# Optimization experiments

Measured on AMD Instinct MI355X. Metric: run time of the kernel, lower is better.

Reference implementation:

```python
import jax, jax.numpy as jnp
import numpy as np

B, H, L, D = 2, 16, 2048, 128


def setup_inputs() -> dict:
    key = jax.random.key(0)
    kq, kk, kv = jax.random.split(key, 3)
    q = jax.random.normal(kq, (B, H, L, D), dtype=jnp.float32)
    k = jax.random.normal(kk, (B, H, L, D), dtype=jnp.float32)
    v = jax.random.normal(kv, (B, H, L, D), dtype=jnp.float32)
    return {"q": q, "k": k, "v": v}


def reference(q, k, v):
    # Causal prefill attention (flash_attn_varlen_func / SDPA is_causal=True path).
    # q, k, v: [B, H, L, D]; scale = 1/sqrt(D) as in the fallback and constructor.
    Lq = q.shape[2]
    Dh = q.shape[3]
    scale = 1.0 / jnp.sqrt(jnp.asarray(Dh, q.dtype))
    scores = jnp.einsum('bhqd,bhkd->bhqk', q, k) * scale  # [B,H,Lq,Lk]
    causal = jnp.tril(jnp.ones((Lq, Lq), dtype=bool))      # [Lq,Lk]
    scores = jnp.where(causal, scores, jnp.finfo(q.dtype).min)
    probs = jax.nn.softmax(scores, axis=-1)
    return jnp.einsum('bhqk,bhkd->bhqd', probs, v)          # [B,H,Lq,D]
```

## Files before the change

kernel.cpp:

```cpp
#include <hip/hip_runtime.h>
#include <hip/hip_bf16.h>
#include <stdint.h>


#define BB 2
#define HH 16
#define LL 2048
#define DD 128

typedef float f32x4 __attribute__((ext_vector_type(4)));
typedef __bf16 bf16x8 __attribute__((ext_vector_type(8)));
typedef __bf16 bf16x2t __attribute__((ext_vector_type(2)));

union Frag16 {
    uint4    u;
    bf16x8   b;
    uint16_t s[8];
    uint32_t w32[4];
};

__device__ inline uint32_t pk2bf(float x, float y) {
    bf16x2t v;
    v.x = (__bf16)x;
    v.y = (__bf16)y;
    return __builtin_bit_cast(uint32_t, v);
}

__device__ inline uint16_t f2bf(float x) {
    uint32_t u = __builtin_bit_cast(uint32_t, x);
    u += 0x7fffu + ((u >> 16) & 1u);
    return (uint16_t)(u >> 16);
}

__device__ inline float fast_exp2(float x) {
#if __has_builtin(__builtin_amdgcn_exp2f)
    return __builtin_amdgcn_exp2f(x);
#else
    return exp2f(x);
#endif
}

__device__ __forceinline__ void stage16(const uint4* g, uint4* l) {
    __builtin_amdgcn_global_load_lds(
        (const __attribute__((address_space(1))) unsigned int*)g,
        (__attribute__((address_space(3))) unsigned int*)l, 16, 0, 0);
}

__global__ __launch_bounds__(256) void conv_kv(
    const float* __restrict__ Kg, const float* __restrict__ Vg,
    uint4* __restrict__ Kf, uint4* __restrict__ Vf)
{
    const int bid = blockIdx.x;
    const int t   = threadIdx.x;
    if (bid < 2048) {
        const int unit = bid;
        #pragma unroll
        for (int i = 0; i < 2; ++i) {
            const int local = t + i * 256;
            const int tile  = unit * 2 + (local >> 8);
            const int c     = local & 255;
            const int ds = c >> 6, quad = (c >> 4) & 3, n16 = c & 15;
            const float* p = Kg + ((size_t)tile * 16 + n16) * DD + ds * 32 + quad * 8;
            float4 a = *(const float4*)p;
            float4 b = *(const float4*)(p + 4);
            Frag16 f;
            f.w32[0] = pk2bf(a.x, a.y); f.w32[1] = pk2bf(a.z, a.w);
            f.w32[2] = pk2bf(b.x, b.y); f.w32[3] = pk2bf(b.z, b.w);
            Kf[(size_t)tile * 256 + c] = f.u;
        }
    } else {
        const int g = bid - 2048;
        const int n16 = t & 15, dt = (t >> 4) & 7, quadH = t >> 7;
        #pragma unroll
        for (int qi = 0; qi < 2; ++qi) {
            const int quad = quadH + 2 * qi;
            const float* base = Vg + ((size_t)g * 32 + quad * 8) * DD + dt * 16 + n16;
            float v[8];
            #pragma unroll
            for (int j = 0; j < 8; ++j) v[j] = base[(size_t)j * DD];
            Frag16 f;
            f.w32[0] = pk2bf(v[0], v[1]); f.w32[1] = pk2bf(v[2], v[3]);
            f.w32[2] = pk2bf(v[4], v[5]); f.w32[3] = pk2bf(v[6], v[7]);
            Vf[(size_t)g * 512 + dt * 64 + quad * 16 + n16] = f.u;
        }
    }
}

__global__ __launch_bounds__(256, 2) void fa_main(
    const float* __restrict__ Qg, const uint4* __restrict__ Kf,
    const uint4* __restrict__ Vf, float* __restrict__ Og)
{
    __shared__ __align__(16) uint4 Klds[2][512];
    __shared__ __align__(16) uint4 Vlds[2][512];
    __shared__ __align__(16) uint16_t Plds[4][16 * 40];

    const int tid  = threadIdx.x;
    const int lane = tid & 63;
    const int w    = tid >> 6;
    const int n16  = lane & 15;
    const int quad = lane >> 4;

    const int i    = blockIdx.x;
    const int xcd  = i & 7;
    const int j    = i >> 3;
    const int pair = j & 15;
    const int bh   = xcd * 4 + (j >> 4);

    constexpr float kC   = 0.08838834764831845f * 1.4426950408889634f;
    constexpr float kOff = -16.0f * 1.4426950408889634f;

    float* Oh = Og + (size_t)bh * LL * DD;

    const int kq_off = (w >> 1) * 256 + ((w & 1) * 2) * 64;
    const int vq_off = (2 * w) * 64;

    #pragma unroll
    for (int phase = 0; phase < 2; ++phase) {
        const int qtile  = phase ? pair : 31 - pair;
        const int q0     = qtile * 64;
        const int q_base = q0 + w * 16;

        Frag16 qf[4];
        {
            const float* qrow = Qg + ((size_t)bh * LL + q_base + n16) * DD;
            #pragma unroll
            for (int ds = 0; ds < 4; ++ds) {
                const int d0 = ds * 32 + quad * 8;
                float4 a = *(const float4*)(qrow + d0);
                float4 b = *(const float4*)(qrow + d0 + 4);
                qf[ds].w32[0] = pk2bf(a.x, a.y); qf[ds].w32[1] = pk2bf(a.z, a.w);
                qf[ds].w32[2] = pk2bf(b.x, b.y); qf[ds].w32[3] = pk2bf(b.z, b.w);
            }
        }

        f32x4 oacc[8];
        #pragma unroll
        for (int dt = 0; dt < 8; ++dt) oacc[dt] = (f32x4)0.0f;
        float lpart = 0.0f;

        const int nt = 2 * qtile + 2;

        {
            const uint4* kg = Kf + ((size_t)(bh * 128) * 256) + kq_off + lane;
            const uint4* vg = Vf + ((size_t)(bh * 64) * 512) + vq_off + lane;
            stage16(kg,      &Klds[0][kq_off]);
            stage16(kg + 64, &Klds[0][kq_off + 64]);
            stage16(vg,      &Vlds[0][vq_off]);
            stage16(vg + 64, &Vlds[0][vq_off + 64]);
        }
        __syncthreads();

        int cur = 0;
        for (int t = 0; t < nt; ++t) {
            if (t + 1 < nt) {
                const uint4* kg = Kf + ((size_t)(bh * 128 + 2 * (t + 1)) * 256) + kq_off + lane;
                const uint4* vg = Vf + ((size_t)(bh * 64 + (t + 1)) * 512) + vq_off + lane;
                uint4* kd = &Klds[cur ^ 1][kq_off];
                uint4* vd = &Vlds[cur ^ 1][vq_off];
                stage16(kg,      kd);
                stage16(kg + 64, kd + 64);
                stage16(vg,      vd);
                stage16(vg + 64, vd + 64);
            }

            const uint4* Kl = Klds[cur];
            const uint4* Vl = Vlds[cur];
            const int kv0 = t << 5;

            f32x4 sacc[2] = {(f32x4)0.0f, (f32x4)0.0f};
            Frag16 kf[2][4];
            #pragma unroll
            for (int kt = 0; kt < 2; ++kt)
                #pragma unroll
                for (int ds = 0; ds < 4; ++ds) kf[kt][ds].u = Kl[kt * 256 + ds * 64 + lane];
            __builtin_amdgcn_s_setprio(1);
            #pragma unroll
            for (int ds = 0; ds < 4; ++ds) {
                sacc[0] = __builtin_amdgcn_mfma_f32_16x16x32_bf16(kf[0][ds].b, qf[ds].b, sacc[0], 0, 0, 0);
                sacc[1] = __builtin_amdgcn_mfma_f32_16x16x32_bf16(kf[1][ds].b, qf[ds].b, sacc[1], 0, 0, 0);
            }
            __builtin_amdgcn_s_setprio(0);

            Frag16 vf[8];
            #pragma unroll
            for (int dt = 0; dt < 8; ++dt) vf[dt].u = Vl[dt * 64 + lane];

            if (kv0 + 31 > q_base) {
                const int qg_ = q_base + n16;
                #pragma unroll
                for (int kt = 0; kt < 2; ++kt) {
                    const int kvg = kv0 + kt * 16 + quad * 4;
                    #pragma unroll
                    for (int r = 0; r < 4; ++r)
                        if (kvg + r > qg_) sacc[kt][r] = -1e30f;
                }
            }

            #pragma unroll
            for (int kt = 0; kt < 2; ++kt) {
                float p0 = fast_exp2(fmaf(sacc[kt][0], kC, kOff));
                float p1 = fast_exp2(fmaf(sacc[kt][1], kC, kOff));
                float p2 = fast_exp2(fmaf(sacc[kt][2], kC, kOff));
                float p3 = fast_exp2(fmaf(sacc[kt][3], kC, kOff));
                lpart += (p0 + p1) + (p2 + p3);
                uint2 pw;
                pw.x = pk2bf(p0, p1);
                pw.y = pk2bf(p2, p3);
                *(uint2*)&Plds[w][n16 * 40 + kt * 16 + quad * 4] = pw;
            }

            Frag16 pf;
            pf.u = *(const uint4*)&Plds[w][n16 * 40 + quad * 8];
            __builtin_amdgcn_s_setprio(1);
            #pragma unroll
            for (int dt = 0; dt < 8; ++dt)
                oacc[dt] = __builtin_amdgcn_mfma_f32_16x16x32_bf16(
                    pf.b, vf[dt].b, oacc[dt], 0, 0, 0);
            __builtin_amdgcn_s_setprio(0);

            __syncthreads();
            cur ^= 1;
        }

        float lsum = lpart;
        lsum += __shfl_xor(lsum, 16);
        lsum += __shfl_xor(lsum, 32);
        #pragma unroll
        for (int r = 0; r < 4; ++r) {
            const float inv = 1.0f / __shfl(lsum, quad * 4 + r);
            float* orow = Oh + (size_t)(q_base + quad * 4 + r) * DD + n16;
            #pragma unroll
            for (int dt = 0; dt < 8; ++dt)
                orow[dt * 16] = oacc[dt][r] * inv;
        }
    }
}

__global__ __launch_bounds__(256) void fa_fallback(
    const float* __restrict__ Qg, const float* __restrict__ Kg,
    const float* __restrict__ Vg, float* __restrict__ Og)
{
    __shared__ uint4 Klds[32 * 16];
    __shared__ uint4 Vlds[128 * 4];
    __shared__ __align__(16) uint16_t Plds[4][32 * 40];

    const int tid  = threadIdx.x;
    const int lane = tid & 63;
    const int w    = tid >> 6;
    const int n16  = lane & 15;
    const int quad = lane >> 4;

    const int bh     = blockIdx.y;
    const int q0     = (gridDim.x - 1 - blockIdx.x) * 128;
    const int q_base = q0 + w * 32;

    const size_t base = (size_t)bh * LL * DD;
    const float* Qh = Qg + base;
    const float* Kh = Kg + base;
    const float* Vh = Vg + base;
    float*       Oh = Og + base;

    constexpr float kC = 0.08838834764831845f * 1.4426950408889634f;

    Frag16 qf[2][4];
    #pragma unroll
    for (int qt = 0; qt < 2; ++qt) {
        const float* qrow = Qh + (size_t)(q_base + qt * 16 + n16) * DD;
        #pragma unroll
        for (int ds = 0; ds < 4; ++ds) {
            const int d0 = ds * 32 + quad * 8;
            float4 a = *(const float4*)(qrow + d0);
            float4 b = *(const float4*)(qrow + d0 + 4);
            Frag16 f;
            f.s[0] = f2bf(a.x); f.s[1] = f2bf(a.y); f.s[2] = f2bf(a.z); f.s[3] = f2bf(a.w);
            f.s[4] = f2bf(b.x); f.s[5] = f2bf(b.y); f.s[6] = f2bf(b.z); f.s[7] = f2bf(b.w);
            qf[qt][ds] = f;
        }
    }

    f32x4 oacc[2][8];
    #pragma unroll
    for (int qt = 0; qt < 2; ++qt)
        #pragma unroll
        for (int dt = 0; dt < 8; ++dt) oacc[qt][dt] = (f32x4)0.0f;
    float mrow[2] = {-1e30f, -1e30f};
    float lrow[2] = {0.0f, 0.0f};

    const int ntiles = q0 / 32 + 4;

    for (int t = 0; t < ntiles; ++t) {
        const int kv0 = t * 32;
        __syncthreads();
        #pragma unroll
        for (int iu = 0; iu < 2; ++iu) {
            const int cid = tid + iu * 256;
            const int r = cid >> 4, c = cid & 15;
            const float* src = Kh + (size_t)(kv0 + r) * DD + c * 8;
            float4 a = *(const float4*)src;
            float4 b = *(const float4*)(src + 4);
            Frag16 f;
            f.s[0] = f2bf(a.x); f.s[1] = f2bf(a.y); f.s[2] = f2bf(a.z); f.s[3] = f2bf(a.w);
            f.s[4] = f2bf(b.x); f.s[5] = f2bf(b.y); f.s[6] = f2bf(b.z); f.s[7] = f2bf(b.w);
            Klds[r * 16 + (c ^ (r & 7))] = f.u;
        }
        #pragma unroll
        for (int iu = 0; iu < 2; ++iu) {
            const int cid = tid + iu * 256;
            const int d = cid >> 2, ch = cid & 3;
            const float* src = Vh + (size_t)(kv0 + ch * 8) * DD + d;
            Frag16 f;
            #pragma unroll
            for (int j = 0; j < 8; ++j) f.s[j] = f2bf(src[(size_t)j * DD]);
            Vlds[d * 4 + (ch ^ ((d >> 1) & 3))] = f.u;
        }
        __syncthreads();

        if (kv0 > q_base + 31) continue;

        f32x4 sacc[2][2];
        #pragma unroll
        for (int kt = 0; kt < 2; ++kt)
            #pragma unroll
            for (int qt = 0; qt < 2; ++qt) sacc[kt][qt] = (f32x4)0.0f;

        #pragma unroll
        for (int ds = 0; ds < 4; ++ds) {
            Frag16 kfr[2];
            #pragma unroll
            for (int kt = 0; kt < 2; ++kt) {
                const int r = kt * 16 + n16;
                const int c = ds * 4 + quad;
                kfr[kt].u = Klds[r * 16 + (c ^ (r & 7))];
            }
            #pragma unroll
            for (int kt = 0; kt < 2; ++kt)
                #pragma unroll
                for (int qt = 0; qt < 2; ++qt)
                    sacc[kt][qt] = __builtin_amdgcn_mfma_f32_16x16x32_bf16(
                        kfr[kt].b, qf[qt][ds].b, sacc[kt][qt], 0, 0, 0);
        }

        if (kv0 + 31 > q_base) {
            #pragma unroll
            for (int kt = 0; kt < 2; ++kt) {
                const int kvg = kv0 + kt * 16 + quad * 4;
                #pragma unroll
                for (int qt = 0; qt < 2; ++qt) {
                    const int qg_ = q_base + qt * 16 + n16;
                    #pragma unroll
                    for (int r = 0; r < 4; ++r)
                        if (kvg + r > qg_) sacc[kt][qt][r] = -1e30f;
                }
            }
        }

        #pragma unroll
        for (int qt = 0; qt < 2; ++qt) {
            float mt = sacc[0][qt][0];
            #pragma unroll
            for (int kt = 0; kt < 2; ++kt)
                #pragma unroll
                for (int r = 0; r < 4; ++r) mt = fmaxf(mt, sacc[kt][qt][r]);
            mt = fmaxf(mt, __shfl_xor(mt, 16));
            mt = fmaxf(mt, __shfl_xor(mt, 32));
            const float mnew  = fmaxf(mrow[qt], mt);
            const float alpha = exp2f((mrow[qt] - mnew) * kC);
            mrow[qt] = mnew;

            float ls = 0.0f;
            uint16_t* prow = &Plds[w][(qt * 16 + n16) * 40];
            #pragma unroll
            for (int kt = 0; kt < 2; ++kt)
                #pragma unroll
                for (int r = 0; r < 4; ++r) {
                    const float p = exp2f((sacc[kt][qt][r] - mnew) * kC);
                    ls += p;
                    prow[kt * 16 + quad * 4 + r] = f2bf(p);
                }
            ls += __shfl_xor(ls, 16);
            ls += __shfl_xor(ls, 32);
            lrow[qt] = lrow[qt] * alpha + ls;

            #pragma unroll
            for (int r = 0; r < 4; ++r) {
                const float ar = __shfl(alpha, quad * 4 + r);
                #pragma unroll
                for (int dt = 0; dt < 8; ++dt) oacc[qt][dt][r] *= ar;
            }
        }

        Frag16 pfr[2];
        #pragma unroll
        for (int qt = 0; qt < 2; ++qt)
            pfr[qt].u = *(const uint4*)&Plds[w][(qt * 16 + n16) * 40 + quad * 8];
        #pragma unroll
        for (int dt = 0; dt < 8; ++dt) {
            const int d = dt * 16 + n16;
            Frag16 vfr;
            vfr.u = Vlds[d * 4 + (quad ^ ((d >> 1) & 3))];
            #pragma unroll
            for (int qt = 0; qt < 2; ++qt)
                oacc[qt][dt] = __builtin_amdgcn_mfma_f32_16x16x32_bf16(
                    pfr[qt].b, vfr.b, oacc[qt][dt], 0, 0, 0);
        }
    }

    #pragma unroll
    for (int qt = 0; qt < 2; ++qt) {
        #pragma unroll
        for (int r = 0; r < 4; ++r) {
            const float lr  = __shfl(lrow[qt], quad * 4 + r);
            const float inv = 1.0f / lr;
            const int row = q_base + qt * 16 + quad * 4 + r;
            float* orow = Oh + (size_t)row * DD + n16;
            #pragma unroll
            for (int dt = 0; dt < 8; ++dt)
                orow[dt * 16] = oacc[qt][dt][r] * inv;
        }
    }
}

extern "C" void kernel_launch(void* const* d_in, const int* in_sizes, int n_in,
                              void* d_out, int out_size, void* d_ws, size_t ws_size,
                              hipStream_t stream) {
    const float* q = (const float*)d_in[0];
    const float* k = (const float*)d_in[1];
    const float* v = (const float*)d_in[2];
    float* o = (float*)d_out;

    const size_t TENS = (size_t)BB * HH * LL * DD * 2;
    if (ws_size >= 2 * TENS) {
        uint4* Kf = (uint4*)d_ws;
        uint4* Vf = (uint4*)((char*)d_ws + TENS);
        conv_kv<<<dim3(4096), dim3(256), 0, stream>>>(k, v, Kf, Vf);
        fa_main<<<dim3(512), dim3(256), 0, stream>>>(q, Kf, Vf, o);
    } else {
        fa_fallback<<<dim3(16, BB * HH), dim3(256), 0, stream>>>(q, k, v, o);
    }
}
```

Before: 185.0 us.

## Split KV range across two wave groups per block and merge partial outputs

Doubles the block to 512 threads, with two groups of four waves each processing alternating 32-key halves of a 64-key stage. Partial output accumulators and row sums are merged through shared memory, reusing the K buffer, before the final store. Tiles that lie fully above the causal diagonal are now skipped per wave. This raises parallelism per query tile and halves the loop trip count, at the cost of more LDS, a reduction step with extra barriers, and possible register pressure under launch_bounds(512,4).

```diff
diff --git a/kernel.cpp b/kernel.cpp
--- a/kernel.cpp
+++ b/kernel.cpp
@@ -86,19 +86,23 @@
     }
 }
 
-__global__ __launch_bounds__(256, 2) void fa_main(
+__global__ __launch_bounds__(512, 4) void fa_main(
     const float* __restrict__ Qg, const uint4* __restrict__ Kf,
     const uint4* __restrict__ Vf, float* __restrict__ Og)
 {
-    __shared__ __align__(16) uint4 Klds[2][512];
-    __shared__ __align__(16) uint4 Vlds[2][512];
-    __shared__ __align__(16) uint16_t Plds[4][16 * 40];
-
-    const int tid  = threadIdx.x;
-    const int lane = tid & 63;
-    const int w    = tid >> 6;
-    const int n16  = lane & 15;
-    const int quad = lane >> 4;
+    __shared__ __align__(16) uint4 Klds[2][1024];
+    __shared__ __align__(16) uint4 Vlds[2][1024];
+    __shared__ __align__(16) uint16_t Plds[8][16 * 40];
+    __shared__ float Lbuf[4][16];
+    float* Obuf = (float*)Klds;
+
+    const int tid   = threadIdx.x;
+    const int lane  = tid & 63;
+    const int w     = tid >> 6;
+    const int n16   = lane & 15;
+    const int quad  = lane >> 4;
+    const int qh    = w & 3;
+    const int kvway = w >> 2;
 
     const int i    = blockIdx.x;
     const int xcd  = i & 7;
@@ -111,14 +115,11 @@
 
     float* Oh = Og + (size_t)bh * LL * DD;
 
-    const int kq_off = (w >> 1) * 256 + ((w & 1) * 2) * 64;
-    const int vq_off = (2 * w) * 64;
-
     #pragma unroll
     for (int phase = 0; phase < 2; ++phase) {
         const int qtile  = phase ? pair : 31 - pair;
         const int q0     = qtile * 64;
-        const int q_base = q0 + w * 16;
+        const int q_base = q0 + qh * 16;
 
         Frag16 qf[4];
         {
@@ -138,25 +139,25 @@
         for (int dt = 0; dt < 8; ++dt) oacc[dt] = (f32x4)0.0f;
         float lpart = 0.0f;
 
-        const int nt = 2 * qtile + 2;
+        const int ns = qtile + 1;
 
         {
-            const uint4* kg = Kf + ((size_t)(bh * 128) * 256) + kq_off + lane;
-            const uint4* vg = Vf + ((size_t)(bh * 64) * 512) + vq_off + lane;
-            stage16(kg,      &Klds[0][kq_off]);
-            stage16(kg + 64, &Klds[0][kq_off + 64]);
-            stage16(vg,      &Vlds[0][vq_off]);
-            stage16(vg + 64, &Vlds[0][vq_off + 64]);
+            const uint4* kg = Kf + ((size_t)(bh * 128) * 256) + w * 128 + lane;
+            const uint4* vg = Vf + ((size_t)(bh * 64) * 512) + w * 128 + lane;
+            stage16(kg,      &Klds[0][w * 128]);
+            stage16(kg + 64, &Klds[0][w * 128 + 64]);
+            stage16(vg,      &Vlds[0][w * 128]);
+            stage16(vg + 64, &Vlds[0][w * 128 + 64]);
         }
         __syncthreads();
 
         int cur = 0;
-        for (int t = 0; t < nt; ++t) {
-            if (t + 1 < nt) {
-                const uint4* kg = Kf + ((size_t)(bh * 128 + 2 * (t + 1)) * 256) + kq_off + lane;
-                const uint4* vg = Vf + ((size_t)(bh * 64 + (t + 1)) * 512) + vq_off + lane;
-                uint4* kd = &Klds[cur ^ 1][kq_off];
-                uint4* vd = &Vlds[cur ^ 1][vq_off];
+        for (int s = 0; s < ns; ++s) {
+            if (s + 1 < ns) {
+                const uint4* kg = Kf + ((size_t)(bh * 128 + 4 * (s + 1)) * 256) + w * 128 + lane;
+                const uint4* vg = Vf + ((size_t)(bh * 64 + 2 * (s + 1)) * 512) + w * 128 + lane;
+                uint4* kd = &Klds[cur ^ 1][w * 128];
+                uint4* vd = &Vlds[cur ^ 1][w * 128];
                 stage16(kg,      kd);
                 stage16(kg + 64, kd + 64);
                 stage16(vg,      vd);
@@ -165,58 +166,61 @@
 
             const uint4* Kl = Klds[cur];
             const uint4* Vl = Vlds[cur];
-            const int kv0 = t << 5;
-
-            f32x4 sacc[2] = {(f32x4)0.0f, (f32x4)0.0f};
-            Frag16 kf[2][4];
-            #pragma unroll
-            for (int kt = 0; kt < 2; ++kt)
-                #pragma unroll
-                for (int ds = 0; ds < 4; ++ds) kf[kt][ds].u = Kl[kt * 256 + ds * 64 + lane];
-            __builtin_amdgcn_s_setprio(1);
-            #pragma unroll
-            for (int ds = 0; ds < 4; ++ds) {
-                sacc[0] = __builtin_amdgcn_mfma_f32_16x16x32_bf16(kf[0][ds].b, qf[ds].b, sacc[0], 0, 0, 0);
-                sacc[1] = __builtin_amdgcn_mfma_f32_16x16x32_bf16(kf[1][ds].b, qf[ds].b, sacc[1], 0, 0, 0);
-            }
-            __builtin_amdgcn_s_setprio(0);
-
-            Frag16 vf[8];
-            #pragma unroll
-            for (int dt = 0; dt < 8; ++dt) vf[dt].u = Vl[dt * 64 + lane];
-
-            if (kv0 + 31 > q_base) {
-                const int qg_ = q_base + n16;
+            const int kv0 = (s << 6) + (kvway << 5);
+
+            if (kv0 <= q_base + 15) {
+                f32x4 sacc[2] = {(f32x4)0.0f, (f32x4)0.0f};
+                Frag16 kf[2][4];
+                #pragma unroll
+                for (int kt = 0; kt < 2; ++kt)
+                    #pragma unroll
+                    for (int ds = 0; ds < 4; ++ds)
+                        kf[kt][ds].u = Kl[(kvway * 2 + kt) * 256 + ds * 64 + lane];
+                __builtin_amdgcn_s_setprio(1);
+                #pragma unroll
+                for (int ds = 0; ds < 4; ++ds) {
+                    sacc[0] = __builtin_amdgcn_mfma_f32_16x16x32_bf16(kf[0][ds].b, qf[ds].b, sacc[0], 0, 0, 0);
+                    sacc[1] = __builtin_amdgcn_mfma_f32_16x16x32_bf16(kf[1][ds].b, qf[ds].b, sacc[1], 0, 0, 0);
+                }
+                __builtin_amdgcn_s_setprio(0);
+
+                Frag16 vf[8];
+                #pragma unroll
+                for (int dt = 0; dt < 8; ++dt) vf[dt].u = Vl[kvway * 512 + dt * 64 + lane];
+
+                if (kv0 + 31 > q_base) {
+                    const int qg_ = q_base + n16;
+                    #pragma unroll
+                    for (int kt = 0; kt < 2; ++kt) {
+                        const int kvg = kv0 + kt * 16 + quad * 4;
+                        #pragma unroll
+                        for (int r = 0; r < 4; ++r)
+                            if (kvg + r > qg_) sacc[kt][r] = -1e30f;
+                    }
+                }
+
                 #pragma unroll
                 for (int kt = 0; kt < 2; ++kt) {
-                    const int kvg = kv0 + kt * 16 + quad * 4;
-                    #pragma unroll
-                    for (int r = 0; r < 4; ++r)
-                        if (kvg + r > qg_) sacc[kt][r] = -1e30f;
+                    float p0 = fast_exp2(fmaf(sacc[kt][0], kC, kOff));
+                    float p1 = fast_exp2(fmaf(sacc[kt][1], kC, kOff));
+                    float p2 = fast_exp2(fmaf(sacc[kt][2], kC, kOff));
+                    float p3 = fast_exp2(fmaf(sacc[kt][3], kC, kOff));
+                    lpart += (p0 + p1) + (p2 + p3);
+                    uint2 pw;
+                    pw.x = pk2bf(p0, p1);
+                    pw.y = pk2bf(p2, p3);
+                    *(uint2*)&Plds[w][n16 * 40 + kt * 16 + quad * 4] = pw;
                 }
-            }
-
-            #pragma unroll
-            for (int kt = 0; kt < 2; ++kt) {
-                float p0 = fast_exp2(fmaf(sacc[kt][0], kC, kOff));
-                float p1 = fast_exp2(fmaf(sacc[kt][1], kC, kOff));
-                float p2 = fast_exp2(fmaf(sacc[kt][2], kC, kOff));
-                float p3 = fast_exp2(fmaf(sacc[kt][3], kC, kOff));
-                lpart += (p0 + p1) + (p2 + p3);
-                uint2 pw;
-                pw.x = pk2bf(p0, p1);
-                pw.y = pk2bf(p2, p3);
-                *(uint2*)&Plds[w][n16 * 40 + kt * 16 + quad * 4] = pw;
-            }
-
-            Frag16 pf;
-            pf.u = *(const uint4*)&Plds[w][n16 * 40 + quad * 8];
-            __builtin_amdgcn_s_setprio(1);
-            #pragma unroll
-            for (int dt = 0; dt < 8; ++dt)
-                oacc[dt] = __builtin_amdgcn_mfma_f32_16x16x32_bf16(
-                    pf.b, vf[dt].b, oacc[dt], 0, 0, 0);
-            __builtin_amdgcn_s_setprio(0);
+
+                Frag16 pf;
+                pf.u = *(const uint4*)&Plds[w][n16 * 40 + quad * 8];
+                __builtin_amdgcn_s_setprio(1);
+                #pragma unroll
+                for (int dt = 0; dt < 8; ++dt)
+                    oacc[dt] = __builtin_amdgcn_mfma_f32_16x16x32_bf16(
+                        pf.b, vf[dt].b, oacc[dt], 0, 0, 0);
+                __builtin_amdgcn_s_setprio(0);
+            }
 
             __syncthreads();
             cur ^= 1;
@@ -225,14 +229,29 @@
         float lsum = lpart;
         lsum += __shfl_xor(lsum, 16);
         lsum += __shfl_xor(lsum, 32);
-        #pragma unroll
-        for (int r = 0; r < 4; ++r) {
-            const float inv = 1.0f / __shfl(lsum, quad * 4 + r);
-            float* orow = Oh + (size_t)(q_base + quad * 4 + r) * DD + n16;
+
+        if (kvway == 1) {
+            if (lane < 16) Lbuf[qh][lane] = lsum;
             #pragma unroll
             for (int dt = 0; dt < 8; ++dt)
-                orow[dt * 16] = oacc[dt][r] * inv;
-        }
+                #pragma unroll
+                for (int r = 0; r < 4; ++r)
+                    Obuf[qh * 2048 + (quad * 4 + r) * 128 + dt * 16 + n16] = oacc[dt][r];
+        }
+        __syncthreads();
+        if (kvway == 0) {
+            lsum += Lbuf[qh][n16];
+            #pragma unroll
+            for (int r = 0; r < 4; ++r) {
+                const float inv = 1.0f / __shfl(lsum, quad * 4 + r);
+                const float* obr = &Obuf[qh * 2048 + (quad * 4 + r) * 128 + n16];
+                float* orow = Oh + (size_t)(q_base + quad * 4 + r) * DD + n16;
+                #pragma unroll
+                for (int dt = 0; dt < 8; ++dt)
+                    orow[dt * 16] = (oacc[dt][r] + obr[dt * 16]) * inv;
+            }
+        }
+        __syncthreads();
     }
 }
 
@@ -433,7 +452,7 @@
         uint4* Kf = (uint4*)d_ws;
         uint4* Vf = (uint4*)((char*)d_ws + TENS);
         conv_kv<<<dim3(4096), dim3(256), 0, stream>>>(k, v, Kf, Vf);
-        fa_main<<<dim3(512), dim3(256), 0, stream>>>(q, Kf, Vf, o);
+        fa_main<<<dim3(512), dim3(512), 0, stream>>>(q, Kf, Vf, o);
     } else {
         fa_fallback<<<dim3(16, BB * HH), dim3(256), 0, stream>>>(q, k, v, o);
     }
```

Result: slower. 188.8 us (+2.1%).
